# Optimization experiments

Measured on AMD Instinct MI355X. Metric: run time of the kernel, lower is better.

Reference implementation:

```python
import jax, jax.numpy as jnp
import numpy as np
import math

D_MODEL = 768
N_HEAD = 12
SEQ_LEN = 2048
BATCH = 4


def setup_inputs() -> dict:
    key = jax.random.key(0)
    ks = jax.random.split(key, 5)
    x = jax.random.normal(ks[0], (BATCH, SEQ_LEN, D_MODEL), dtype=jnp.float32)
    s = 1.0 / math.sqrt(D_MODEL)
    W_attn = jax.random.uniform(ks[1], (D_MODEL, 3 * D_MODEL), minval=-s, maxval=s, dtype=jnp.float32)
    b_attn = jax.random.uniform(ks[2], (3 * D_MODEL,), minval=-s, maxval=s, dtype=jnp.float32)
    W_proj = jax.random.uniform(ks[3], (D_MODEL, D_MODEL), minval=-s, maxval=s, dtype=jnp.float32)
    b_proj = jax.random.uniform(ks[4], (D_MODEL,), minval=-s, maxval=s, dtype=jnp.float32)
    return {"x": x, "W_attn": W_attn, "b_attn": b_attn, "W_proj": W_proj, "b_proj": b_proj}


def reference(x, W_attn, b_attn, W_proj, b_proj):
    B, T, C = x.shape
    H = N_HEAD
    hd = C // H
    qkv = x @ W_attn + b_attn  # [B,T,3C]
    q, k, v = jnp.split(qkv, 3, axis=-1)
    # [B,H,T,hd]
    q = q.reshape(B, T, H, hd).transpose(0, 2, 1, 3)
    k = k.reshape(B, T, H, hd).transpose(0, 2, 1, 3)
    v = v.reshape(B, T, H, hd).transpose(0, 2, 1, 3)
    att = jnp.einsum('bhqd,bhkd->bhqk', q, k) * (1.0 / math.sqrt(hd))  # [B,H,T,T]
    causal = jnp.tril(jnp.ones((T, T), dtype=bool))
    att = jnp.where(causal[None, None, :, :], att, -jnp.inf)
    att = jax.nn.softmax(att, axis=-1)
    # attn_pdrop = resid_pdrop = 0.0 -> dropout is identity
    y = jnp.einsum('bhqk,bhkd->bhqd', att, v)  # [B,H,T,hd]
    y = y.transpose(0, 2, 1, 3).reshape(B, T, C)
    return y @ W_proj + b_proj
```

## Files before the change

### kernel.cpp

```cpp
#include <hip/hip_runtime.h>
#include <hip/hip_bf16.h>
#include <math.h>

#define D_MODEL 768
#define N_HEAD  12
#define SEQ     2048
#define BATCH   4
#define HD      64
#define BH      (BATCH*N_HEAD)

typedef __bf16 bf16;
typedef __bf16 bf16x4 __attribute__((ext_vector_type(4)));
typedef __bf16 bf16x8 __attribute__((ext_vector_type(8)));
typedef float  f32x4  __attribute__((ext_vector_type(4)));
typedef float  f32x16 __attribute__((ext_vector_type(16)));
typedef unsigned int u32;

__device__ __forceinline__ f32x4 mfma16(bf16x8 a, bf16x8 b, f32x4 c) {
    return __builtin_amdgcn_mfma_f32_16x16x32_bf16(a, b, c, 0, 0, 0);
}
__device__ __forceinline__ f32x16 mfma32(bf16x8 a, bf16x8 b, f32x16 c) {
    return __builtin_amdgcn_mfma_f32_32x32x16_bf16(a, b, c, 0, 0, 0);
}

__device__ __forceinline__ void gload16(const void* g, void* l) {
    __builtin_amdgcn_global_load_lds((const __attribute__((address_space(1))) u32*)g,
                                     (__attribute__((address_space(3))) u32*)l, 16, 0, 0);
}

__global__ __launch_bounds__(256)
void prep(const float* __restrict__ x, const float* __restrict__ Wa, const float* __restrict__ Wp,
          bf16* __restrict__ xb, bf16* __restrict__ Wab, bf16* __restrict__ Wpb) {
    __shared__ float tile[64][65];
    int blk = blockIdx.x, tid = threadIdx.x;
    if (blk < 6144) {
        int i = (blk * 256 + tid) * 4;
        float4 v = *(const float4*)(x + i);
        bf16x4 o;
        o[0] = (bf16)v.x; o[1] = (bf16)v.y; o[2] = (bf16)v.z; o[3] = (bf16)v.w;
        *(bf16x4*)(xb + i) = o;
        return;
    }
    const float* in; bf16* out; int C; int tile_id;
    if (blk < 6576) { in = Wa; out = Wab; C = 2304; tile_id = blk - 6144; }
    else            { in = Wp; out = Wpb; C = 768;  tile_id = blk - 6576; }
    const int R = 768;
    int tpr = C / 64;
    int tr = (tile_id / tpr) * 64, tc = (tile_id % tpr) * 64;
    int r0 = tid >> 4, c0 = (tid & 15) * 4;
    #pragma unroll
    for (int i = 0; i < 4; ++i) {
        float4 v = *(const float4*)&in[(long)(tr + r0 + i * 16) * C + tc + c0];
        tile[r0 + i * 16][c0 + 0] = v.x;
        tile[r0 + i * 16][c0 + 1] = v.y;
        tile[r0 + i * 16][c0 + 2] = v.z;
        tile[r0 + i * 16][c0 + 3] = v.w;
    }
    __syncthreads();
    int orr = (tid & 15) * 4;
    #pragma unroll
    for (int i = 0; i < 4; ++i) {
        int oc = (tid >> 4) + i * 16;
        bf16x4 o;
        #pragma unroll
        for (int j = 0; j < 4; ++j) o[j] = (bf16)tile[orr + j][oc];
        *(bf16x4*)&out[(long)(tc + oc) * R + tr + orr] = o;
    }
}

template<int MODE>
__global__ __launch_bounds__(256)
void gemm_bt(const bf16* __restrict__ A, const bf16* __restrict__ Bt,
             const float* __restrict__ bias,
             bf16* __restrict__ qo, bf16* __restrict__ ko, bf16* __restrict__ vto,
             float* __restrict__ outf,
             int M, int N, int K) {
    __shared__ bf16 As[128 * 64];
    __shared__ bf16 Bs[128 * 64];
    int tid = threadIdx.x;
    int wave = tid >> 6, lane = tid & 63;
    int wr = wave >> 1, wc = wave & 1;
    int lq = lane >> 4, lc = lane & 15;
    int mbase = blockIdx.x * 128, nbase = blockIdx.y * 128;
    int srow = wave * 32 + (lane >> 3);
    int scol = ((lane & 7) ^ (lane >> 3)) << 3;
    const bf16* aS = A  + (long)(mbase + srow) * K + scol;
    const bf16* bS = Bt + (long)(nbase + srow) * K + scol;
    char* AsB = (char*)As + wave * 4096;
    char* BsB = (char*)Bs + wave * 4096;
    f32x4 acc[4][4] = {};
    for (int kt = 0; kt < K; kt += 64) {
        #pragma unroll
        for (int j = 0; j < 4; ++j) {
            gload16(aS + kt + (long)j * 8 * K, AsB + j * 1024);
            gload16(bS + kt + (long)j * 8 * K, BsB + j * 1024);
        }
        __syncthreads();
        #pragma unroll
        for (int ksub = 0; ksub < 2; ++ksub) {
            bf16x8 af[4], bfr[4];
            #pragma unroll
            for (int mf = 0; mf < 4; ++mf) {
                int R = wr * 64 + mf * 16 + lc;
                af[mf]  = *(const bf16x8*)((char*)As + R * 128 + (((ksub * 4 + lq) ^ (lc & 7)) << 4));
            }
            #pragma unroll
            for (int nf = 0; nf < 4; ++nf) {
                int R = wc * 64 + nf * 16 + lc;
                bfr[nf] = *(const bf16x8*)((char*)Bs + R * 128 + (((ksub * 4 + lq) ^ (lc & 7)) << 4));
            }
            __builtin_amdgcn_s_setprio(1);
            #pragma unroll
            for (int mf = 0; mf < 4; ++mf)
                #pragma unroll
                for (int nf = 0; nf < 4; ++nf)
                    acc[mf][nf] = mfma16(af[mf], bfr[nf], acc[mf][nf]);
            __builtin_amdgcn_s_setprio(0);
        }
        __syncthreads();
    }
    #pragma unroll
    for (int mf = 0; mf < 4; ++mf) {
        #pragma unroll
        for (int nf = 0; nf < 4; ++nf) {
            int n = nbase + wc * 64 + nf * 16 + lc;
            float bv = bias[n];
            int m0 = mbase + wr * 64 + mf * 16 + lq * 4;
            if (MODE == 0) {
                int sect = n / 768, cc = n % 768;
                int h = cc >> 6, d = cc & 63;
                int b = m0 >> 11, t0 = m0 & 2047;
                long bh = (long)b * N_HEAD + h;
                if (sect == 0) {
                    #pragma unroll
                    for (int r = 0; r < 4; ++r)
                        qo[(bh * SEQ + t0 + r) * HD + d] = (bf16)((acc[mf][nf][r] + bv) * 0.18033688f);
                } else if (sect == 1) {
                    #pragma unroll
                    for (int r = 0; r < 4; ++r)
                        ko[(bh * SEQ + t0 + r) * HD + d] = (bf16)(acc[mf][nf][r] + bv);
                } else {
                    bf16x4 o;
                    #pragma unroll
                    for (int r = 0; r < 4; ++r) o[r] = (bf16)(acc[mf][nf][r] + bv);
                    *(bf16x4*)&vto[(bh * HD + d) * SEQ + t0] = o;
                }
            } else {
                #pragma unroll
                for (int r = 0; r < 4; ++r)
                    outf[(long)(m0 + r) * N + n] = acc[mf][nf][r] + bv;
            }
        }
    }
}

__global__ __launch_bounds__(256, 4)
void attn_kernel(const bf16* __restrict__ qg, const bf16* __restrict__ kg,
                 const bf16* __restrict__ vtg, bf16* __restrict__ yg) {
    __shared__ __align__(16) bf16 KV[4][64 * 64];
    int tid = threadIdx.x;
    int wave = tid >> 6, lane = tid & 63;
    int q5 = lane & 31, h = lane >> 5;
    int bh = blockIdx.x;
    int tau = gridDim.y - 1 - blockIdx.y;
    int b = bh / N_HEAD, hh = bh % N_HEAD;
    int rh = wave & 1, wp = wave >> 1;
    int nkt  = tau + 1;
    int half = nkt >> 1;
    int base = wp ? half : 0;
    int cnt  = wp ? nkt - half : half;
    int maxc = nkt - half;
    long koff = (long)bh * SEQ * HD;
    long voff = (long)bh * HD * SEQ;
    int qrow = tau * 64 + rh * 32 + q5;

    bf16x8 qf[4];
    #pragma unroll
    for (int s = 0; s < 4; ++s)
        qf[s] = *(const bf16x8*)&qg[koff + (long)qrow * HD + s * 16 + h * 8];

    f32x16 y0 = {}, y1 = {};
    float m2 = -INFINITY, lsum = 0.f;

    int srow0 = rh * 32 + (lane >> 3);
    int scolsw = ((lane & 7) ^ (lane >> 3)) << 3;
    int rsw = lane & 7;
    const char* KsC = (const char*)KV[2 * wp];
    const char* VsC = (const char*)KV[2 * wp + 1];

    for (int i = 0; i < maxc; ++i) {
        int tt = base + i;
        bool active = i < cnt;
        if (active) {
            int k0 = tt * 64;
            char* KsB = (char*)KV[2 * wp]     + rh * 4096;
            char* VsB = (char*)KV[2 * wp + 1] + rh * 4096;
            #pragma unroll
            for (int j = 0; j < 4; ++j) {
                gload16(kg + koff + (long)(k0 + srow0 + j * 8) * HD + scolsw,  KsB + j * 1024);
                gload16(vtg + voff + (long)(srow0 + j * 8) * SEQ + k0 + scolsw, VsB + j * 1024);
            }
        }
        __syncthreads();
        if (active) {
            int k0 = tt * 64;
            f32x16 s0 = {}, s1 = {};
            __builtin_amdgcn_s_setprio(1);
            #pragma unroll
            for (int s = 0; s < 4; ++s) {
                bf16x8 kf0 = *(const bf16x8*)(KsC + q5 * 128        + (((s * 2 + h) ^ rsw) << 4));
                bf16x8 kf1 = *(const bf16x8*)(KsC + (32 + q5) * 128 + (((s * 2 + h) ^ rsw) << 4));
                s0 = mfma32(kf0, qf[s], s0);
                s1 = mfma32(kf1, qf[s], s1);
            }
            __builtin_amdgcn_s_setprio(0);
            if (tt == nkt - 1) {
                #pragma unroll
                for (int r = 0; r < 16; ++r) {
                    int ka = k0 + (r & 3) + 8 * (r >> 2) + 4 * h;
                    if (ka > qrow)      s0[r] = -INFINITY;
                    if (ka + 32 > qrow) s1[r] = -INFINITY;
                }
            }
            float pmax = s0[0];
            #pragma unroll
            for (int r = 1; r < 16; ++r) pmax = fmaxf(pmax, s0[r]);
            #pragma unroll
            for (int r = 0; r < 16; ++r) pmax = fmaxf(pmax, s1[r]);
            pmax = fmaxf(pmax, __shfl_xor(pmax, 32));
            if (!__all(pmax <= m2 + 11.5f)) {
                float mnew = fmaxf(m2, pmax);
                float sc = __builtin_amdgcn_exp2f(m2 - mnew);
                #pragma unroll
                for (int r = 0; r < 16; ++r) { y0[r] *= sc; y1[r] *= sc; }
                lsum *= sc;
                m2 = mnew;
            }
            float psum = 0.f;
            u32 d0a[4], d1a[4], d0b[4], d1b[4];
            #pragma unroll
            for (int m = 0; m < 4; ++m) {
                union { bf16x4 v; u32 w[2]; } pa, pb;
                #pragma unroll
                for (int rr = 0; rr < 4; ++rr) {
                    float p0 = __builtin_amdgcn_exp2f(s0[4 * m + rr] - m2);
                    float p1 = __builtin_amdgcn_exp2f(s1[4 * m + rr] - m2);
                    psum += p0 + p1;
                    pa.v[rr] = (bf16)p0; pb.v[rr] = (bf16)p1;
                }
                d0a[m] = pa.w[0]; d1a[m] = pa.w[1];
                d0b[m] = pb.w[0]; d1b[m] = pb.w[1];
            }
            psum += __shfl_xor(psum, 32);
            lsum += psum;
            u32 e0a[4], e1a[4], e0b[4], e1b[4];
            #pragma unroll
            for (int m = 0; m < 4; ++m) {
                e0a[m] = __shfl_xor(d0a[m], 32); e1a[m] = __shfl_xor(d1a[m], 32);
                e0b[m] = __shfl_xor(d0b[m], 32); e1b[m] = __shfl_xor(d1b[m], 32);
            }
            __builtin_amdgcn_s_setprio(1);
            #pragma unroll
            for (int s = 0; s < 4; ++s) {
                int m0 = 2 * (s & 1), m1 = m0 + 1;
                union { bf16x8 v; u32 w[4]; } fr;
                if (s < 2) {
                    fr.w[0] = h ? e0a[m1] : d0a[m0];
                    fr.w[1] = h ? e1a[m1] : d1a[m0];
                    fr.w[2] = h ? d0a[m1] : e0a[m0];
                    fr.w[3] = h ? d1a[m1] : e1a[m0];
                } else {
                    fr.w[0] = h ? e0b[m1] : d0b[m0];
                    fr.w[1] = h ? e1b[m1] : d1b[m0];
                    fr.w[2] = h ? d0b[m1] : e0b[m0];
                    fr.w[3] = h ? d1b[m1] : e1b[m0];
                }
                bf16x8 v0 = *(const bf16x8*)(VsC + q5 * 128        + (((s * 2 + h) ^ rsw) << 4));
                bf16x8 v1 = *(const bf16x8*)(VsC + (32 + q5) * 128 + (((s * 2 + h) ^ rsw) << 4));
                y0 = mfma32(v0, fr.v, y0);
                y1 = mfma32(v1, fr.v, y1);
            }
            __builtin_amdgcn_s_setprio(0);
        }
        __syncthreads();
    }

    float* ms = (float*)&KV[0][0];
    int slot = (rh * 64 + lane) * 36;
    if (wp) {
        ms[slot] = m2; ms[slot + 1] = lsum;
        #pragma unroll
        for (int r = 0; r < 16; ++r) { ms[slot + 4 + r] = y0[r]; ms[slot + 20 + r] = y1[r]; }
    }
    __syncthreads();
    if (!wp) {
        float mB = ms[slot], lB = ms[slot + 1];
        float mf = fmaxf(m2, mB);
        float a  = __builtin_amdgcn_exp2f(m2 - mf);
        float bb = __builtin_amdgcn_exp2f(mB - mf);
        float inv = 1.f / (lsum * a + lB * bb);
        long rowoff = ((long)b * SEQ + qrow) * D_MODEL + (long)hh * HD;
        #pragma unroll
        for (int m = 0; m < 4; ++m) {
            bf16x4 o0, o1;
            #pragma unroll
            for (int rr = 0; rr < 4; ++rr) {
                o0[rr] = (bf16)((y0[4 * m + rr] * a + ms[slot + 4 + 4 * m + rr] * bb) * inv);
                o1[rr] = (bf16)((y1[4 * m + rr] * a + ms[slot + 20 + 4 * m + rr] * bb) * inv);
            }
            *(bf16x4*)&yg[rowoff + 8 * m + 4 * h]      = o0;
            *(bf16x4*)&yg[rowoff + 32 + 8 * m + 4 * h] = o1;
        }
    }
}

extern "C" void kernel_launch(void* const* d_in, const int* in_sizes, int n_in,
                              void* d_out, int out_size, void* d_ws, size_t ws_size,
                              hipStream_t stream) {
    const float* x      = (const float*)d_in[0];
    const float* W_attn = (const float*)d_in[1];
    const float* b_attn = (const float*)d_in[2];
    const float* W_proj = (const float*)d_in[3];
    const float* b_proj = (const float*)d_in[4];
    float* out = (float*)d_out;

    char* ws = (char*)d_ws;
    size_t off = 0;
    auto alloc = [&](size_t bytes) { void* p = ws + off; off += (bytes + 255) & ~255ULL; return p; };
    bf16* xb  = (bf16*)alloc(8192ULL * 768 * 2);
    bf16* Wab = (bf16*)alloc(2304ULL * 768 * 2);
    bf16* Wpb = (bf16*)alloc(768ULL * 768 * 2);
    bf16* qb_ = (bf16*)alloc((size_t)BH * SEQ * HD * 2);
    bf16* kb_ = (bf16*)alloc((size_t)BH * SEQ * HD * 2);
    bf16* vtb = (bf16*)alloc((size_t)BH * SEQ * HD * 2);
    bf16* yb  = (bf16*)alloc(8192ULL * 768 * 2);

    hipLaunchKernelGGL(prep, dim3(6720), dim3(256), 0, stream,
                       x, W_attn, W_proj, xb, Wab, Wpb);
    hipLaunchKernelGGL((gemm_bt<0>), dim3(64, 18), dim3(256), 0, stream,
                       xb, Wab, b_attn, qb_, kb_, vtb, (float*)nullptr, 8192, 2304, 768);
    hipLaunchKernelGGL(attn_kernel, dim3(48, 32), dim3(256), 0, stream,
                       qb_, kb_, vtb, yb);
    hipLaunchKernelGGL((gemm_bt<1>), dim3(64, 6), dim3(256), 0, stream,
                       yb, Wpb, b_proj, (bf16*)nullptr, (bf16*)nullptr, (bf16*)nullptr, out, 8192, 768, 768);
}
```

Before: 191.7 us.

## Load K and V fragments directly from global memory, dropping LDS staging

The attention loop no longer stages K and V tiles through shared memory with per-iteration block barriers. Each wave now loads its MFMA operand fragments straight from global memory into registers, and the V loads are issued before the softmax work so they can overlap it. Shared memory is kept only for the final cross-wave merge, with a 37-float stride to reduce bank conflicts. This removes the two __syncthreads per tile and the idle iterations caused by unequal key-split counts. In exchange it costs more global and L2 traffic, since the two row-half waves reload the same K/V, and more registers are live.

Result: slower. 262.6 us (+37.0%).

```diff
diff --git a/kernel.cpp b/kernel.cpp
--- a/kernel.cpp
+++ b/kernel.cpp
@@ -157,7 +157,7 @@
 __global__ __launch_bounds__(256, 4)
 void attn_kernel(const bf16* __restrict__ qg, const bf16* __restrict__ kg,
                  const bf16* __restrict__ vtg, bf16* __restrict__ yg) {
-    __shared__ __align__(16) bf16 KV[4][64 * 64];
+    __shared__ float ms[128 * 37];
     int tid = threadIdx.x;
     int wave = tid >> 6, lane = tid & 63;
     int q5 = lane & 31, h = lane >> 5;
@@ -169,7 +169,6 @@
     int half = nkt >> 1;
     int base = wp ? half : 0;
     int cnt  = wp ? nkt - half : half;
-    int maxc = nkt - half;
     long koff = (long)bh * SEQ * HD;
     long voff = (long)bh * HD * SEQ;
     int qrow = tau * 64 + rh * 32 + q5;
@@ -182,115 +181,103 @@
     f32x16 y0 = {}, y1 = {};
     float m2 = -INFINITY, lsum = 0.f;
 
-    int srow0 = rh * 32 + (lane >> 3);
-    int scolsw = ((lane & 7) ^ (lane >> 3)) << 3;
-    int rsw = lane & 7;
-    const char* KsC = (const char*)KV[2 * wp];
-    const char* VsC = (const char*)KV[2 * wp + 1];
-
-    for (int i = 0; i < maxc; ++i) {
+    for (int i = 0; i < cnt; ++i) {
         int tt = base + i;
-        bool active = i < cnt;
-        if (active) {
-            int k0 = tt * 64;
-            char* KsB = (char*)KV[2 * wp]     + rh * 4096;
-            char* VsB = (char*)KV[2 * wp + 1] + rh * 4096;
-            #pragma unroll
-            for (int j = 0; j < 4; ++j) {
-                gload16(kg + koff + (long)(k0 + srow0 + j * 8) * HD + scolsw,  KsB + j * 1024);
-                gload16(vtg + voff + (long)(srow0 + j * 8) * SEQ + k0 + scolsw, VsB + j * 1024);
-            }
-        }
-        __syncthreads();
-        if (active) {
-            int k0 = tt * 64;
-            f32x16 s0 = {}, s1 = {};
-            __builtin_amdgcn_s_setprio(1);
-            #pragma unroll
-            for (int s = 0; s < 4; ++s) {
-                bf16x8 kf0 = *(const bf16x8*)(KsC + q5 * 128        + (((s * 2 + h) ^ rsw) << 4));
-                bf16x8 kf1 = *(const bf16x8*)(KsC + (32 + q5) * 128 + (((s * 2 + h) ^ rsw) << 4));
-                s0 = mfma32(kf0, qf[s], s0);
-                s1 = mfma32(kf1, qf[s], s1);
-            }
-            __builtin_amdgcn_s_setprio(0);
-            if (tt == nkt - 1) {
-                #pragma unroll
-                for (int r = 0; r < 16; ++r) {
-                    int ka = k0 + (r & 3) + 8 * (r >> 2) + 4 * h;
-                    if (ka > qrow)      s0[r] = -INFINITY;
-                    if (ka + 32 > qrow) s1[r] = -INFINITY;
-                }
-            }
-            float pmax = s0[0];
-            #pragma unroll
-            for (int r = 1; r < 16; ++r) pmax = fmaxf(pmax, s0[r]);
-            #pragma unroll
-            for (int r = 0; r < 16; ++r) pmax = fmaxf(pmax, s1[r]);
-            pmax = fmaxf(pmax, __shfl_xor(pmax, 32));
-            if (!__all(pmax <= m2 + 11.5f)) {
-                float mnew = fmaxf(m2, pmax);
-                float sc = __builtin_amdgcn_exp2f(m2 - mnew);
-                #pragma unroll
-                for (int r = 0; r < 16; ++r) { y0[r] *= sc; y1[r] *= sc; }
-                lsum *= sc;
-                m2 = mnew;
-            }
-            float psum = 0.f;
-            u32 d0a[4], d1a[4], d0b[4], d1b[4];
-            #pragma unroll
-            for (int m = 0; m < 4; ++m) {
-                union { bf16x4 v; u32 w[2]; } pa, pb;
-                #pragma unroll
-                for (int rr = 0; rr < 4; ++rr) {
-                    float p0 = __builtin_amdgcn_exp2f(s0[4 * m + rr] - m2);
-                    float p1 = __builtin_amdgcn_exp2f(s1[4 * m + rr] - m2);
-                    psum += p0 + p1;
-                    pa.v[rr] = (bf16)p0; pb.v[rr] = (bf16)p1;
-                }
-                d0a[m] = pa.w[0]; d1a[m] = pa.w[1];
-                d0b[m] = pb.w[0]; d1b[m] = pb.w[1];
-            }
-            psum += __shfl_xor(psum, 32);
-            lsum += psum;
-            u32 e0a[4], e1a[4], e0b[4], e1b[4];
-            #pragma unroll
-            for (int m = 0; m < 4; ++m) {
-                e0a[m] = __shfl_xor(d0a[m], 32); e1a[m] = __shfl_xor(d1a[m], 32);
-                e0b[m] = __shfl_xor(d0b[m], 32); e1b[m] = __shfl_xor(d1b[m], 32);
-            }
-            __builtin_amdgcn_s_setprio(1);
-            #pragma unroll
-            for (int s = 0; s < 4; ++s) {
-                int m0 = 2 * (s & 1), m1 = m0 + 1;
-                union { bf16x8 v; u32 w[4]; } fr;
-                if (s < 2) {
-                    fr.w[0] = h ? e0a[m1] : d0a[m0];
-                    fr.w[1] = h ? e1a[m1] : d1a[m0];
-                    fr.w[2] = h ? d0a[m1] : e0a[m0];
-                    fr.w[3] = h ? d1a[m1] : e1a[m0];
-                } else {
-                    fr.w[0] = h ? e0b[m1] : d0b[m0];
-                    fr.w[1] = h ? e1b[m1] : d1b[m0];
-                    fr.w[2] = h ? d0b[m1] : e0b[m0];
-                    fr.w[3] = h ? d1b[m1] : e1b[m0];
-                }
-                bf16x8 v0 = *(const bf16x8*)(VsC + q5 * 128        + (((s * 2 + h) ^ rsw) << 4));
-                bf16x8 v1 = *(const bf16x8*)(VsC + (32 + q5) * 128 + (((s * 2 + h) ^ rsw) << 4));
-                y0 = mfma32(v0, fr.v, y0);
-                y1 = mfma32(v1, fr.v, y1);
-            }
-            __builtin_amdgcn_s_setprio(0);
-        }
-        __syncthreads();
-    }
-
-    float* ms = (float*)&KV[0][0];
-    int slot = (rh * 64 + lane) * 36;
+        int k0 = tt * 64;
+        const bf16* kp = kg + koff + (long)k0 * HD;
+        const bf16* vp = vtg + voff + k0;
+        bf16x8 kf0[4], kf1[4];
+        #pragma unroll
+        for (int s = 0; s < 4; ++s) {
+            kf0[s] = *(const bf16x8*)(kp + (long)q5 * HD + s * 16 + h * 8);
+            kf1[s] = *(const bf16x8*)(kp + (long)(32 + q5) * HD + s * 16 + h * 8);
+        }
+        f32x16 s0 = {}, s1 = {};
+        __builtin_amdgcn_s_setprio(1);
+        #pragma unroll
+        for (int s = 0; s < 4; ++s) {
+            s0 = mfma32(kf0[s], qf[s], s0);
+            s1 = mfma32(kf1[s], qf[s], s1);
+        }
+        __builtin_amdgcn_s_setprio(0);
+        bf16x8 v0[4], v1[4];
+        #pragma unroll
+        for (int s = 0; s < 4; ++s) {
+            v0[s] = *(const bf16x8*)(vp + (long)q5 * SEQ + s * 16 + h * 8);
+            v1[s] = *(const bf16x8*)(vp + (long)(32 + q5) * SEQ + s * 16 + h * 8);
+        }
+        if (tt == nkt - 1) {
+            #pragma unroll
+            for (int r = 0; r < 16; ++r) {
+                int ka = k0 + (r & 3) + 8 * (r >> 2) + 4 * h;
+                if (ka > qrow)      s0[r] = -INFINITY;
+                if (ka + 32 > qrow) s1[r] = -INFINITY;
+            }
+        }
+        float pmax = s0[0];
+        #pragma unroll
+        for (int r = 1; r < 16; ++r) pmax = fmaxf(pmax, s0[r]);
+        #pragma unroll
+        for (int r = 0; r < 16; ++r) pmax = fmaxf(pmax, s1[r]);
+        pmax = fmaxf(pmax, __shfl_xor(pmax, 32));
+        if (!__all(pmax <= m2 + 11.5f)) {
+            float mnew = fmaxf(m2, pmax);
+            float sc = __builtin_amdgcn_exp2f(m2 - mnew);
+            #pragma unroll
+            for (int r = 0; r < 16; ++r) { y0[r] *= sc; y1[r] *= sc; }
+            lsum *= sc;
+            m2 = mnew;
+        }
+        float psum = 0.f;
+        u32 d0a[4], d1a[4], d0b[4], d1b[4];
+        #pragma unroll
+        for (int m = 0; m < 4; ++m) {
+            union { bf16x4 v; u32 w[2]; } pa, pb;
+            #pragma unroll
+            for (int rr = 0; rr < 4; ++rr) {
+                float p0 = __builtin_amdgcn_exp2f(s0[4 * m + rr] - m2);
+                float p1 = __builtin_amdgcn_exp2f(s1[4 * m + rr] - m2);
+                psum += p0 + p1;
+                pa.v[rr] = (bf16)p0; pb.v[rr] = (bf16)p1;
+            }
+            d0a[m] = pa.w[0]; d1a[m] = pa.w[1];
+            d0b[m] = pb.w[0]; d1b[m] = pb.w[1];
+        }
+        psum += __shfl_xor(psum, 32);
+        lsum += psum;
+        u32 e0a[4], e1a[4], e0b[4], e1b[4];
+        #pragma unroll
+        for (int m = 0; m < 4; ++m) {
+            e0a[m] = __shfl_xor(d0a[m], 32); e1a[m] = __shfl_xor(d1a[m], 32);
+            e0b[m] = __shfl_xor(d0b[m], 32); e1b[m] = __shfl_xor(d1b[m], 32);
+        }
+        __builtin_amdgcn_s_setprio(1);
+        #pragma unroll
+        for (int s = 0; s < 4; ++s) {
+            int m0 = 2 * (s & 1), m1 = m0 + 1;
+            union { bf16x8 v; u32 w[4]; } fr;
+            if (s < 2) {
+                fr.w[0] = h ? e0a[m1] : d0a[m0];
+                fr.w[1] = h ? e1a[m1] : d1a[m0];
+                fr.w[2] = h ? d0a[m1] : e0a[m0];
+                fr.w[3] = h ? d1a[m1] : e1a[m0];
+            } else {
+                fr.w[0] = h ? e0b[m1] : d0b[m0];
+                fr.w[1] = h ? e1b[m1] : d1b[m0];
+                fr.w[2] = h ? d0b[m1] : e0b[m0];
+                fr.w[3] = h ? d1b[m1] : e1b[m0];
+            }
+            y0 = mfma32(v0[s], fr.v, y0);
+            y1 = mfma32(v1[s], fr.v, y1);
+        }
+        __builtin_amdgcn_s_setprio(0);
+    }
+
+    int slot = (rh * 64 + lane) * 37;
     if (wp) {
         ms[slot] = m2; ms[slot + 1] = lsum;
         #pragma unroll
-        for (int r = 0; r < 16; ++r) { ms[slot + 4 + r] = y0[r]; ms[slot + 20 + r] = y1[r]; }
+        for (int r = 0; r < 16; ++r) { ms[slot + 2 + r] = y0[r]; ms[slot + 18 + r] = y1[r]; }
     }
     __syncthreads();
     if (!wp) {
@@ -305,8 +292,8 @@
             bf16x4 o0, o1;
             #pragma unroll
             for (int rr = 0; rr < 4; ++rr) {
-                o0[rr] = (bf16)((y0[4 * m + rr] * a + ms[slot + 4 + 4 * m + rr] * bb) * inv);
-                o1[rr] = (bf16)((y1[4 * m + rr] * a + ms[slot + 20 + 4 * m + rr] * bb) * inv);
+                o0[rr] = (bf16)((y0[4 * m + rr] * a + ms[slot + 2 + 4 * m + rr] * bb) * inv);
+                o1[rr] = (bf16)((y1[4 * m + rr] * a + ms[slot + 18 + 4 * m + rr] * bb) * inv);
             }
             *(bf16x4*)&yg[rowoff + 8 * m + 4 * h]      = o0;
             *(bf16x4*)&yg[rowoff + 32 + 8 * m + 4 * h] = o1;
```
